# Performance work log

Hardware: AMD Instinct MI355X
Metric: run time of the kernel (lower is better)

Reference implementation:

```python
import jax, jax.numpy as jnp
import numpy as np
import math

N_HEADS = 16
D_EFF = 64
ROPE_BASE = 500.0


def _rope(x, cos, sin):
    # x: (b, h, L, d_eff); cos/sin: (L, d_eff//2)
    x_even = x[..., 0::2]
    x_odd = x[..., 1::2]
    rot = jnp.stack([x_even * cos - x_odd * sin,
                     x_even * sin + x_odd * cos], axis=-1)
    return rot.reshape(x.shape)


def setup_inputs() -> dict:
    key = jax.random.key(0)
    ks = jax.random.split(key, 5)
    B, L, D = 1, 2048, 1024
    X = jax.random.normal(ks[0], (B, L, D), dtype=jnp.float32)
    # causal mask (1 = keep, 0 = masked), broadcastable to (B, h, L, L)
    mask = jnp.tril(jnp.ones((L, L), dtype=jnp.int32))[None, :, :]
    s = 1.0 / math.sqrt(D)
    Wq = jax.random.normal(ks[1], (D, D), dtype=jnp.float32) * s
    Wk = jax.random.normal(ks[2], (D, D), dtype=jnp.float32) * s
    Wv = jax.random.normal(ks[3], (D, D), dtype=jnp.float32) * s
    Wo = jax.random.normal(ks[4], (D, D), dtype=jnp.float32) * s
    return {"X": X, "mask": mask, "Wq": Wq, "Wk": Wk, "Wv": Wv, "Wo": Wo}


def reference(X, mask, Wq, Wk, Wv, Wo):
    b, L, d_model = X.shape
    h, d = N_HEADS, D_EFF
    d_full = h * d

    def split_heads(Y):
        return Y.reshape(b, L, h, d).transpose(0, 2, 1, 3)  # (b,h,L,d)

    Q = split_heads(X @ Wq)
    K = split_heads(X @ Wk)
    V = split_heads(X @ Wv)

    # interleaved RoPE, base 500
    inv_freq = 1.0 / (ROPE_BASE ** (jnp.arange(0, d, 2, dtype=jnp.float32) / d))
    freqs = jnp.arange(L, dtype=jnp.float32)[:, None] * inv_freq  # (L, d/2)
    cos, sin = jnp.cos(freqs), jnp.sin(freqs)
    Q = _rope(Q, cos, sin)
    K = _rope(K, cos, sin)

    S = jnp.einsum('bhqd,bhkd->bhqk', Q, K) / math.sqrt(d)
    S = jnp.where(mask[:, None, :, :] == 0, jnp.float32(-1e9), S)
    # NOTE: faithful to original torch code: softmax over the HEADS axis (dim=1)
    A = jax.nn.softmax(S, axis=1)
    Y = jnp.einsum('bhqk,bhkd->bhqd', A, V)
    Y = Y.transpose(0, 2, 1, 3).reshape(b, L, d_full)
    Y = Y @ Wo
    return Y * math.sqrt(d_model / d_full)
```

## Files before the change

kernel.cpp:

```cpp
#include <hip/hip_runtime.h>
#include <stdint.h>
#include <stddef.h>

typedef __attribute__((ext_vector_type(8))) short bf16x8;
typedef __attribute__((ext_vector_type(4))) short short4v;
typedef __attribute__((ext_vector_type(4))) float f32x4;

__device__ __forceinline__ short f2bf(float f) {
  union { float f; uint32_t u; } x; x.f = f;
  return (short)((x.u + 0x7fffu + ((x.u >> 16) & 1u)) >> 16);
}
__device__ __forceinline__ float bf2f(short s) {
  union { uint32_t u; float f; } x; x.u = ((uint32_t)(uint16_t)s) << 16;
  return x.f;
}

__device__ __forceinline__ void gload_lds16(const void* g, void* lds) {
  __builtin_amdgcn_global_load_lds(
      (const __attribute__((address_space(1))) void*)g,
      (__attribute__((address_space(3))) void*)lds, 16, 0, 0);
}

__global__ __launch_bounds__(256) void cast_b(const float* __restrict__ s,
                                              short* __restrict__ d) {
  int i4 = (blockIdx.x * 256 + threadIdx.x) * 4;
  float4 v = *(const float4*)&s[i4];
  short4v r = { f2bf(v.x), f2bf(v.y), f2bf(v.z), f2bf(v.w) };
  *(short4v*)&d[i4] = r;
}

__global__ __launch_bounds__(256) void cast_add4(const short* __restrict__ Y0,
                                                 const short* __restrict__ Y1,
                                                 const short* __restrict__ Y2,
                                                 const short* __restrict__ Y3,
                                                 const float* __restrict__ Cvs,
                                                 short* __restrict__ o) {
  int i4 = (blockIdx.x * 256 + threadIdx.x) * 4;
  short4v a = *(const short4v*)&Y0[i4];
  short4v b = *(const short4v*)&Y1[i4];
  short4v c = *(const short4v*)&Y2[i4];
  short4v d = *(const short4v*)&Y3[i4];
  short4v r;
#pragma unroll
  for (int j = 0; j < 4; j++) {
    float s = bf2f(a[j]) + bf2f(b[j]) + bf2f(c[j]) + bf2f(d[j]) +
              Cvs[(i4 + j) & 1023];
    r[j] = f2bf(s);
  }
  *(short4v*)&o[i4] = r;
}

__global__ __launch_bounds__(256) void transW(const float* __restrict__ Wq,
                                              const float* __restrict__ Wk,
                                              const float* __restrict__ Wv,
                                              const float* __restrict__ Wo,
                                              short* __restrict__ WcatT,
                                              short* __restrict__ WoT) {
  int z = blockIdx.z;
  const float* src = (z == 0) ? Wq : (z == 1) ? Wk : (z == 2) ? Wv : Wo;
  short* dst = (z == 3) ? WoT : WcatT + (size_t)z * 1024 * 1024;
  __shared__ float tl[32][33];
  int tx = threadIdx.x & 31, ty = threadIdx.x >> 5;
  int kk0 = blockIdx.x * 32;
  int nn0 = blockIdx.y * 32;
#pragma unroll
  for (int j = 0; j < 4; j++)
    tl[ty + j * 8][tx] = src[(size_t)(kk0 + ty + j * 8) * 1024 + nn0 + tx];
  __syncthreads();
#pragma unroll
  for (int j = 0; j < 4; j++)
    dst[(size_t)(nn0 + ty + j * 8) * 1024 + kk0 + tx] = f2bf(tl[tx][ty + j * 8]);
}

__global__ __launch_bounds__(256) void transpose_v(const short* __restrict__ Vb,
                                                   short* __restrict__ Vt) {
  __shared__ short tv[64][72];
  int h = blockIdx.y, k0 = blockIdx.x * 64;
  int tid = threadIdx.x;
#pragma unroll
  for (int j = 0; j < 2; j++) {
    int idx = tid + j * 256;
    int row = idx >> 3, c = idx & 7;
    bf16x8 v = *(const bf16x8*)&Vb[((size_t)h * 2048 + k0 + row) * 64 + c * 8];
#pragma unroll
    for (int t = 0; t < 8; t++) tv[row][c * 8 + t] = v[t];
  }
  __syncthreads();
#pragma unroll
  for (int j = 0; j < 2; j++) {
    int idx = tid + j * 256;
    int d = idx >> 3, c = idx & 7;
    bf16x8 v;
#pragma unroll
    for (int t = 0; t < 8; t++) v[t] = tv[c * 8 + t][d];
    *(bf16x8*)&Vt[((size_t)h * 64 + d) * 2048 + k0 + c * 8] = v;
  }
}

__global__ __launch_bounds__(256) void vsum(const short* __restrict__ Vb,
                                            float* __restrict__ Cvs) {
  __shared__ float red[16][17];
  int h = blockIdx.x >> 2, dq = blockIdx.x & 3;
  int dl = threadIdx.x & 15, ks = threadIdx.x >> 4;
  int d = dq * 16 + dl;
  float acc = 0.f;
  const short* base = &Vb[((size_t)h * 2048 + ks * 128) * 64 + d];
#pragma unroll 8
  for (int k = 0; k < 128; k++) acc += bf2f(base[(size_t)k * 64]);
  red[dl][ks] = acc;
  __syncthreads();
  if (threadIdx.x < 16) {
    float sum = 0.f;
#pragma unroll
    for (int i = 0; i < 16; i++) sum += red[threadIdx.x][i];
    Cvs[h * 64 + dq * 16 + threadIdx.x] = sum * 0.0625f;
  }
}

template <int MODE>
__global__ __launch_bounds__(256, 2)
void gemm_kernel(const short* __restrict__ A, const short* __restrict__ B,
                 int N, int K, float* __restrict__ C,
                 short* __restrict__ Qb, short* __restrict__ Kb,
                 short* __restrict__ Vb) {
  __shared__ __attribute__((aligned(16))) short lga[128 * 64];
  __shared__ __attribute__((aligned(16))) short lgb[128 * 64];
  const int tid = threadIdx.x;
  const int lane = tid & 63;
  const int w = tid >> 6;
  const int l15 = lane & 15;
  const int quad = lane >> 4;
  const int wm = w >> 1, wn = w & 1;
  const int m0 = blockIdx.x * 128, n0 = blockIdx.y * 128;
  const int rsub = lane >> 3;
  const int cpos = lane & 7;

  f32x4 acc[4][4];
#pragma unroll
  for (int i = 0; i < 4; i++)
#pragma unroll
    for (int j = 0; j < 4; j++) acc[i][j] = (f32x4){0.f, 0.f, 0.f, 0.f};

  for (int kb = 0; kb < K; kb += 64) {
    __syncthreads();
#pragma unroll
    for (int j = 0; j < 4; j++) {
      int r = (w * 4 + j) * 8 + rsub;
      int kc = cpos ^ rsub;
      gload_lds16(A + (size_t)(m0 + r) * K + kb + kc * 8, &lga[(w * 4 + j) * 512]);
      gload_lds16(B + (size_t)(n0 + r) * K + kb + kc * 8, &lgb[(w * 4 + j) * 512]);
    }
    __syncthreads();
#pragma unroll
    for (int kk = 0; kk < 2; kk++) {
      bf16x8 af[4], bfr[4];
#pragma unroll
      for (int t = 0; t < 4; t++) {
        int row = wm * 64 + t * 16 + l15;
        int pc = (kk * 4 + quad) ^ (row & 7);
        af[t] = *(const bf16x8*)&lga[row * 64 + pc * 8];
        int rowb = wn * 64 + t * 16 + l15;
        int pcb = (kk * 4 + quad) ^ (rowb & 7);
        bfr[t] = *(const bf16x8*)&lgb[rowb * 64 + pcb * 8];
      }
#pragma unroll
      for (int mt = 0; mt < 4; mt++)
#pragma unroll
        for (int nt = 0; nt < 4; nt++)
          acc[mt][nt] = __builtin_amdgcn_mfma_f32_16x16x32_bf16(
              af[mt], bfr[nt], acc[mt][nt], 0, 0, 0);
    }
  }

  if (MODE == 0) {
#pragma unroll
    for (int mt = 0; mt < 4; mt++) {
      int q = m0 + wm * 64 + mt * 16 + quad * 4;
#pragma unroll
      for (int nt = 0; nt < 4; nt++) {
        int n = n0 + wn * 64 + nt * 16 + l15;
#pragma unroll
        for (int r = 0; r < 4; r++) C[(size_t)(q + r) * N + n] = acc[mt][nt][r];
      }
    }
  } else {
#pragma unroll
    for (int mt = 0; mt < 4; mt++) {
#pragma unroll
      for (int nt = 0; nt < 4; nt++) {
        int n = n0 + wn * 64 + nt * 16 + l15;
        int mat = n >> 10;
        int h = (n >> 6) & 15;
        int d = n & 63;
#pragma unroll
        for (int r = 0; r < 4; r++) {
          int q = m0 + wm * 64 + mt * 16 + quad * 4 + r;
          float v = acc[mt][nt][r];
          float o = __shfl_xor(v, 1, 64);
          if (mat < 2) {
            int i = d >> 1;
            float ang = (float)q * __builtin_exp2f(-(float)i * 0.2801807588956902f);
            float sn, cs;
            __sincosf(ang, &sn, &cs);
            float rv = (d & 1) ? (o * sn + v * cs) : (v * cs - o * sn);
            short* dst = (mat == 0) ? Qb : Kb;
            dst[((size_t)h * 2048 + q) * 64 + d] = f2bf(rv);
          } else {
            Vb[((size_t)h * 2048 + q) * 64 + d] = f2bf(v);
          }
        }
      }
    }
  }
}

__global__ __launch_bounds__(512, 4)
void attn_kernel(const short* __restrict__ Qb, const short* __restrict__ Kb,
                 const short* __restrict__ Vt, short* __restrict__ Yp) {
  __shared__ short Sb[16 * 16 * 72];
  __shared__ short Ab[16 * 16 * 72];
  const int tid = threadIdx.x;
  const int lane = tid & 63;
  const int w = tid >> 6;
  const int l15 = lane & 15, quad = lane >> 4;
  const int bx = blockIdx.x;
  const int qt = 127 - (bx >> 2);
  const int s = bx & 3;
  const int q0 = qt * 16;
  const int G = (qt + 4) >> 2;
  const int h0 = w * 2;

  bf16x8 qf[2][2];
#pragma unroll
  for (int hh = 0; hh < 2; hh++)
#pragma unroll
    for (int c = 0; c < 2; c++)
      qf[hh][c] = *(const bf16x8*)&Qb[((size_t)(h0 + hh) * 2048 + q0 + l15) * 64 +
                                      c * 32 + quad * 8];

  f32x4 yacc[2][4];
#pragma unroll
  for (int i = 0; i < 2; i++)
#pragma unroll
    for (int j = 0; j < 4; j++) yacc[i][j] = (f32x4){0.f, 0.f, 0.f, 0.f};

  for (int g = s; g < G; g += 4) {
    const int k0 = g * 64;
#pragma unroll
    for (int hh = 0; hh < 2; hh++) {
      int h = h0 + hh;
#pragma unroll
      for (int st = 0; st < 4; st++) {
        const short* kb = &Kb[((size_t)h * 2048 + k0 + st * 16 + l15) * 64 + quad * 8];
        bf16x8 kf0 = *(const bf16x8*)kb;
        bf16x8 kf1 = *(const bf16x8*)(kb + 32);
        f32x4 sa = (f32x4){0.f, 0.f, 0.f, 0.f};
        sa = __builtin_amdgcn_mfma_f32_16x16x32_bf16(qf[hh][0], kf0, sa, 0, 0, 0);
        sa = __builtin_amdgcn_mfma_f32_16x16x32_bf16(qf[hh][1], kf1, sa, 0, 0, 0);
#pragma unroll
        for (int r = 0; r < 4; r++)
          Sb[(h * 16 + quad * 4 + r) * 72 + st * 16 + l15] = f2bf(0.125f * sa[r]);
      }
    }
    __syncthreads();
#pragma unroll
    for (int pp = 0; pp < 2; pp++) {
      int p = tid + pp * 512;
      int q = p >> 6, kl = p & 63;
      int base = q * 72 + kl;
      float t[16];
      float m = -1e30f;
#pragma unroll
      for (int h = 0; h < 16; h++) {
        t[h] = bf2f(Sb[h * 1152 + base]);
        m = fmaxf(m, t[h]);
      }
      float sum = 0.f;
#pragma unroll
      for (int h = 0; h < 16; h++) {
        float e = __expf(t[h] - m);
        t[h] = e;
        sum += e;
      }
      float rs = 1.f / sum;
      bool msk = (k0 + kl) > (q0 + q);
#pragma unroll
      for (int h = 0; h < 16; h++)
        Ab[h * 1152 + base] = msk ? (short)0 : f2bf(t[h] * rs - 0.0625f);
    }
    __syncthreads();
#pragma unroll
    for (int hh = 0; hh < 2; hh++) {
      int h = h0 + hh;
#pragma unroll
      for (int kk = 0; kk < 2; kk++) {
        bf16x8 af = *(const bf16x8*)&Ab[(h * 16 + l15) * 72 + kk * 32 + quad * 8];
#pragma unroll
        for (int nt = 0; nt < 4; nt++) {
          bf16x8 vf = *(const bf16x8*)&Vt[((size_t)h * 64 + nt * 16 + l15) * 2048 +
                                          k0 + kk * 32 + quad * 8];
          yacc[hh][nt] = __builtin_amdgcn_mfma_f32_16x16x32_bf16(af, vf, yacc[hh][nt],
                                                                 0, 0, 0);
        }
      }
    }
    __syncthreads();
  }
  short* Y = Yp + (size_t)s * 2048 * 1024;
#pragma unroll
  for (int hh = 0; hh < 2; hh++) {
#pragma unroll
    for (int nt = 0; nt < 4; nt++) {
      int col = (h0 + hh) * 64 + nt * 16 + l15;
#pragma unroll
      for (int r = 0; r < 4; r++)
        Y[(size_t)(q0 + quad * 4 + r) * 1024 + col] = f2bf(yacc[hh][nt][r]);
    }
  }
}

extern "C" void kernel_launch(void* const* d_in, const int* in_sizes, int n_in,
                              void* d_out, int out_size, void* d_ws, size_t ws_size,
                              hipStream_t stream) {
  (void)in_sizes; (void)n_in; (void)out_size; (void)ws_size;
  const float* X  = (const float*)d_in[0];
  const float* Wq = (const float*)d_in[2];
  const float* Wk = (const float*)d_in[3];
  const float* Wv = (const float*)d_in[4];
  const float* Wo = (const float*)d_in[5];
  char* ws = (char*)d_ws;
  const size_t MB = 1024 * 1024;
  short* Xbf   = (short*)(ws + 0);
  short* WcatT = (short*)(ws + 4 * MB);
  short* WoT   = (short*)(ws + 10 * MB);
  short* Qb    = (short*)(ws + 12 * MB);
  short* Kb    = (short*)(ws + 16 * MB);
  short* Vb    = (short*)(ws + 20 * MB);
  short* Vt    = (short*)(ws + 24 * MB);
  short* Yp    = (short*)(ws + 28 * MB);
  float* Cvs   = (float*)(ws + 44 * MB);
  short* Ycbf  = Xbf;
  float* out   = (float*)d_out;

  cast_b<<<dim3(2048), dim3(256), 0, stream>>>(X, Xbf);
  transW<<<dim3(32, 32, 4), dim3(256), 0, stream>>>(Wq, Wk, Wv, Wo, WcatT, WoT);
  gemm_kernel<1><<<dim3(16, 24), dim3(256), 0, stream>>>(Xbf, WcatT, 3072, 1024,
                                                         nullptr, Qb, Kb, Vb);
  transpose_v<<<dim3(32, 16), dim3(256), 0, stream>>>(Vb, Vt);
  vsum<<<dim3(64), dim3(256), 0, stream>>>(Vb, Cvs);
  attn_kernel<<<dim3(512), dim3(512), 0, stream>>>(Qb, Kb, Vt, Yp);
  cast_add4<<<dim3(2048), dim3(256), 0, stream>>>(Yp, Yp + 2048 * 1024,
                                                  Yp + 2 * 2048 * 1024,
                                                  Yp + 3 * 2048 * 1024, Cvs, Ycbf);
  gemm_kernel<0><<<dim3(16, 8), dim3(256), 0, stream>>>(Ycbf, WoT, 1024, 1024,
                                                        out, nullptr, nullptr, nullptr);
}
```

Baseline: 235.4 us.

## Use one wave per head in attention, exp2 softmax, smaller Wo GEMM tiles

The attention kernel now runs 1024 threads with one wave per head, so each thread handles one (query,key) softmax position. The probabilities are written back into the score buffer, removing the second LDS array. The softmax drops the max subtraction and uses exp2 with log2e folded into the score scale, which risks overflow if scores grow large. The output projection GEMM is templated to use 64-row M tiles, doubling the block count for better CU coverage on the small GEMM.

```diff
diff --git a/kernel.cpp b/kernel.cpp
--- a/kernel.cpp
+++ b/kernel.cpp
@@ -117,13 +117,15 @@
   }
 }
 
-template <int MODE>
-__global__ __launch_bounds__(256, 2)
+template <int MODE, int TM>
+__global__ __launch_bounds__(256, TM == 128 ? 2 : 4)
 void gemm_kernel(const short* __restrict__ A, const short* __restrict__ B,
                  int N, int K, float* __restrict__ C,
                  short* __restrict__ Qb, short* __restrict__ Kb,
                  short* __restrict__ Vb) {
-  __shared__ __attribute__((aligned(16))) short lga[128 * 64];
+  constexpr int MT = TM / 32;
+  constexpr int MSUB = TM / 2;
+  __shared__ __attribute__((aligned(16))) short lga[TM * 64];
   __shared__ __attribute__((aligned(16))) short lgb[128 * 64];
   const int tid = threadIdx.x;
   const int lane = tid & 63;
@@ -131,40 +133,50 @@
   const int l15 = lane & 15;
   const int quad = lane >> 4;
   const int wm = w >> 1, wn = w & 1;
-  const int m0 = blockIdx.x * 128, n0 = blockIdx.y * 128;
+  const int m0 = blockIdx.x * TM, n0 = blockIdx.y * 128;
   const int rsub = lane >> 3;
   const int cpos = lane & 7;
 
-  f32x4 acc[4][4];
-#pragma unroll
-  for (int i = 0; i < 4; i++)
+  f32x4 acc[MT][4];
+#pragma unroll
+  for (int i = 0; i < MT; i++)
 #pragma unroll
     for (int j = 0; j < 4; j++) acc[i][j] = (f32x4){0.f, 0.f, 0.f, 0.f};
 
   for (int kb = 0; kb < K; kb += 64) {
     __syncthreads();
 #pragma unroll
+    for (int j = 0; j < TM / 32; j++) {
+      int ci = w * (TM / 32) + j;
+      int r = ci * 8 + rsub;
+      int kc = cpos ^ rsub;
+      gload_lds16(A + (size_t)(m0 + r) * K + kb + kc * 8, &lga[ci * 512]);
+    }
+#pragma unroll
     for (int j = 0; j < 4; j++) {
-      int r = (w * 4 + j) * 8 + rsub;
+      int ci = w * 4 + j;
+      int r = ci * 8 + rsub;
       int kc = cpos ^ rsub;
-      gload_lds16(A + (size_t)(m0 + r) * K + kb + kc * 8, &lga[(w * 4 + j) * 512]);
-      gload_lds16(B + (size_t)(n0 + r) * K + kb + kc * 8, &lgb[(w * 4 + j) * 512]);
+      gload_lds16(B + (size_t)(n0 + r) * K + kb + kc * 8, &lgb[ci * 512]);
     }
     __syncthreads();
 #pragma unroll
     for (int kk = 0; kk < 2; kk++) {
-      bf16x8 af[4], bfr[4];
-#pragma unroll
-      for (int t = 0; t < 4; t++) {
-        int row = wm * 64 + t * 16 + l15;
+      bf16x8 af[MT], bfr[4];
+#pragma unroll
+      for (int t = 0; t < MT; t++) {
+        int row = wm * MSUB + t * 16 + l15;
         int pc = (kk * 4 + quad) ^ (row & 7);
         af[t] = *(const bf16x8*)&lga[row * 64 + pc * 8];
+      }
+#pragma unroll
+      for (int t = 0; t < 4; t++) {
         int rowb = wn * 64 + t * 16 + l15;
         int pcb = (kk * 4 + quad) ^ (rowb & 7);
         bfr[t] = *(const bf16x8*)&lgb[rowb * 64 + pcb * 8];
       }
 #pragma unroll
-      for (int mt = 0; mt < 4; mt++)
+      for (int mt = 0; mt < MT; mt++)
 #pragma unroll
         for (int nt = 0; nt < 4; nt++)
           acc[mt][nt] = __builtin_amdgcn_mfma_f32_16x16x32_bf16(
@@ -174,8 +186,8 @@
 
   if (MODE == 0) {
 #pragma unroll
-    for (int mt = 0; mt < 4; mt++) {
-      int q = m0 + wm * 64 + mt * 16 + quad * 4;
+    for (int mt = 0; mt < MT; mt++) {
+      int q = m0 + wm * MSUB + mt * 16 + quad * 4;
 #pragma unroll
       for (int nt = 0; nt < 4; nt++) {
         int n = n0 + wn * 64 + nt * 16 + l15;
@@ -185,7 +197,7 @@
     }
   } else {
 #pragma unroll
-    for (int mt = 0; mt < 4; mt++) {
+    for (int mt = 0; mt < MT; mt++) {
 #pragma unroll
       for (int nt = 0; nt < 4; nt++) {
         int n = n0 + wn * 64 + nt * 16 + l15;
@@ -194,7 +206,7 @@
         int d = n & 63;
 #pragma unroll
         for (int r = 0; r < 4; r++) {
-          int q = m0 + wm * 64 + mt * 16 + quad * 4 + r;
+          int q = m0 + wm * MSUB + mt * 16 + quad * 4 + r;
           float v = acc[mt][nt][r];
           float o = __shfl_xor(v, 1, 64);
           if (mat < 2) {
@@ -214,108 +226,82 @@
   }
 }
 
-__global__ __launch_bounds__(512, 4)
+__global__ __launch_bounds__(1024, 8)
 void attn_kernel(const short* __restrict__ Qb, const short* __restrict__ Kb,
                  const short* __restrict__ Vt, short* __restrict__ Yp) {
   __shared__ short Sb[16 * 16 * 72];
-  __shared__ short Ab[16 * 16 * 72];
   const int tid = threadIdx.x;
   const int lane = tid & 63;
-  const int w = tid >> 6;
+  const int h = tid >> 6;
   const int l15 = lane & 15, quad = lane >> 4;
   const int bx = blockIdx.x;
   const int qt = 127 - (bx >> 2);
   const int s = bx & 3;
   const int q0 = qt * 16;
   const int G = (qt + 4) >> 2;
-  const int h0 = w * 2;
-
-  bf16x8 qf[2][2];
-#pragma unroll
-  for (int hh = 0; hh < 2; hh++)
-#pragma unroll
-    for (int c = 0; c < 2; c++)
-      qf[hh][c] = *(const bf16x8*)&Qb[((size_t)(h0 + hh) * 2048 + q0 + l15) * 64 +
-                                      c * 32 + quad * 8];
-
-  f32x4 yacc[2][4];
-#pragma unroll
-  for (int i = 0; i < 2; i++)
-#pragma unroll
-    for (int j = 0; j < 4; j++) yacc[i][j] = (f32x4){0.f, 0.f, 0.f, 0.f};
+
+  bf16x8 qf[2];
+#pragma unroll
+  for (int c = 0; c < 2; c++)
+    qf[c] = *(const bf16x8*)&Qb[((size_t)h * 2048 + q0 + l15) * 64 + c * 32 + quad * 8];
+
+  f32x4 yacc[4];
+#pragma unroll
+  for (int j = 0; j < 4; j++) yacc[j] = (f32x4){0.f, 0.f, 0.f, 0.f};
+
+  const int sq = tid >> 6;
+  const int sbase = sq * 72 + lane;
 
   for (int g = s; g < G; g += 4) {
     const int k0 = g * 64;
 #pragma unroll
-    for (int hh = 0; hh < 2; hh++) {
-      int h = h0 + hh;
-#pragma unroll
-      for (int st = 0; st < 4; st++) {
-        const short* kb = &Kb[((size_t)h * 2048 + k0 + st * 16 + l15) * 64 + quad * 8];
-        bf16x8 kf0 = *(const bf16x8*)kb;
-        bf16x8 kf1 = *(const bf16x8*)(kb + 32);
-        f32x4 sa = (f32x4){0.f, 0.f, 0.f, 0.f};
-        sa = __builtin_amdgcn_mfma_f32_16x16x32_bf16(qf[hh][0], kf0, sa, 0, 0, 0);
-        sa = __builtin_amdgcn_mfma_f32_16x16x32_bf16(qf[hh][1], kf1, sa, 0, 0, 0);
-#pragma unroll
-        for (int r = 0; r < 4; r++)
-          Sb[(h * 16 + quad * 4 + r) * 72 + st * 16 + l15] = f2bf(0.125f * sa[r]);
-      }
-    }
-    __syncthreads();
-#pragma unroll
-    for (int pp = 0; pp < 2; pp++) {
-      int p = tid + pp * 512;
-      int q = p >> 6, kl = p & 63;
-      int base = q * 72 + kl;
-      float t[16];
-      float m = -1e30f;
-#pragma unroll
-      for (int h = 0; h < 16; h++) {
-        t[h] = bf2f(Sb[h * 1152 + base]);
-        m = fmaxf(m, t[h]);
-      }
+    for (int st = 0; st < 4; st++) {
+      const short* kb = &Kb[((size_t)h * 2048 + k0 + st * 16 + l15) * 64 + quad * 8];
+      bf16x8 kf0 = *(const bf16x8*)kb;
+      bf16x8 kf1 = *(const bf16x8*)(kb + 32);
+      f32x4 sa = (f32x4){0.f, 0.f, 0.f, 0.f};
+      sa = __builtin_amdgcn_mfma_f32_16x16x32_bf16(qf[0], kf0, sa, 0, 0, 0);
+      sa = __builtin_amdgcn_mfma_f32_16x16x32_bf16(qf[1], kf1, sa, 0, 0, 0);
+#pragma unroll
+      for (int r = 0; r < 4; r++)
+        Sb[h * 1152 + (quad * 4 + r) * 72 + st * 16 + l15] =
+            f2bf(sa[r] * 0.1803368801f);
+    }
+    __syncthreads();
+    {
+      bool msk = (k0 + lane) > (q0 + sq);
+      float e[16];
       float sum = 0.f;
 #pragma unroll
-      for (int h = 0; h < 16; h++) {
-        float e = __expf(t[h] - m);
-        t[h] = e;
-        sum += e;
+      for (int hh = 0; hh < 16; hh++) {
+        e[hh] = __builtin_exp2f(bf2f(Sb[hh * 1152 + sbase]));
+        sum += e[hh];
       }
       float rs = 1.f / sum;
-      bool msk = (k0 + kl) > (q0 + q);
-#pragma unroll
-      for (int h = 0; h < 16; h++)
-        Ab[h * 1152 + base] = msk ? (short)0 : f2bf(t[h] * rs - 0.0625f);
-    }
-    __syncthreads();
-#pragma unroll
-    for (int hh = 0; hh < 2; hh++) {
-      int h = h0 + hh;
-#pragma unroll
-      for (int kk = 0; kk < 2; kk++) {
-        bf16x8 af = *(const bf16x8*)&Ab[(h * 16 + l15) * 72 + kk * 32 + quad * 8];
-#pragma unroll
-        for (int nt = 0; nt < 4; nt++) {
-          bf16x8 vf = *(const bf16x8*)&Vt[((size_t)h * 64 + nt * 16 + l15) * 2048 +
-                                          k0 + kk * 32 + quad * 8];
-          yacc[hh][nt] = __builtin_amdgcn_mfma_f32_16x16x32_bf16(af, vf, yacc[hh][nt],
-                                                                 0, 0, 0);
-        }
+#pragma unroll
+      for (int hh = 0; hh < 16; hh++)
+        Sb[hh * 1152 + sbase] = msk ? (short)0 : f2bf(e[hh] * rs - 0.0625f);
+    }
+    __syncthreads();
+#pragma unroll
+    for (int kk = 0; kk < 2; kk++) {
+      bf16x8 af = *(const bf16x8*)&Sb[(h * 16 + l15) * 72 + kk * 32 + quad * 8];
+#pragma unroll
+      for (int nt = 0; nt < 4; nt++) {
+        bf16x8 vf = *(const bf16x8*)&Vt[((size_t)h * 64 + nt * 16 + l15) * 2048 +
+                                        k0 + kk * 32 + quad * 8];
+        yacc[nt] = __builtin_amdgcn_mfma_f32_16x16x32_bf16(af, vf, yacc[nt], 0, 0, 0);
       }
     }
     __syncthreads();
   }
   short* Y = Yp + (size_t)s * 2048 * 1024;
 #pragma unroll
-  for (int hh = 0; hh < 2; hh++) {
-#pragma unroll
-    for (int nt = 0; nt < 4; nt++) {
-      int col = (h0 + hh) * 64 + nt * 16 + l15;
-#pragma unroll
-      for (int r = 0; r < 4; r++)
-        Y[(size_t)(q0 + quad * 4 + r) * 1024 + col] = f2bf(yacc[hh][nt][r]);
-    }
+  for (int nt = 0; nt < 4; nt++) {
+    int col = h * 64 + nt * 16 + l15;
+#pragma unroll
+    for (int r = 0; r < 4; r++)
+      Y[(size_t)(q0 + quad * 4 + r) * 1024 + col] = f2bf(yacc[nt][r]);
   }
 }
 
@@ -344,14 +330,14 @@
 
   cast_b<<<dim3(2048), dim3(256), 0, stream>>>(X, Xbf);
   transW<<<dim3(32, 32, 4), dim3(256), 0, stream>>>(Wq, Wk, Wv, Wo, WcatT, WoT);
-  gemm_kernel<1><<<dim3(16, 24), dim3(256), 0, stream>>>(Xbf, WcatT, 3072, 1024,
-                                                         nullptr, Qb, Kb, Vb);
+  gemm_kernel<1, 128><<<dim3(16, 24), dim3(256), 0, stream>>>(
+      Xbf, WcatT, 3072, 1024, nullptr, Qb, Kb, Vb);
   transpose_v<<<dim3(32, 16), dim3(256), 0, stream>>>(Vb, Vt);
   vsum<<<dim3(64), dim3(256), 0, stream>>>(Vb, Cvs);
-  attn_kernel<<<dim3(512), dim3(512), 0, stream>>>(Qb, Kb, Vt, Yp);
+  attn_kernel<<<dim3(512), dim3(1024), 0, stream>>>(Qb, Kb, Vt, Yp);
   cast_add4<<<dim3(2048), dim3(256), 0, stream>>>(Yp, Yp + 2048 * 1024,
                                                   Yp + 2 * 2048 * 1024,
                                                   Yp + 3 * 2048 * 1024, Cvs, Ycbf);
-  gemm_kernel<0><<<dim3(16, 8), dim3(256), 0, stream>>>(Ycbf, WoT, 1024, 1024,
-                                                        out, nullptr, nullptr, nullptr);
-}
+  gemm_kernel<0, 64><<<dim3(32, 8), dim3(256), 0, stream>>>(
+      Ycbf, WoT, 1024, 1024, out, nullptr, nullptr, nullptr);
+}
```

Result: no change. 235.6 us (+0.1%).
